# Kernel optimization log

Hardware: AMD Instinct MI355X
Metric: run time of the kernel (lower is better)

Reference implementation:

```python
import jax, jax.numpy as jnp
import numpy as np

N, C, H, W = 4, 256, 64, 64
D = 128  # inter_channels = C // 2


def setup_inputs() -> dict:
    key = jax.random.key(0)
    ks = jax.random.split(key, 9)
    s = 0.05  # weight scale
    return {
        "x": jax.random.normal(ks[0], (N, C, H, W), jnp.float32),
        "Wg": jax.random.normal(ks[1], (D, C), jnp.float32) * s,
        "bg": jax.random.normal(ks[2], (D,), jnp.float32) * s,
        "Wt": jax.random.normal(ks[3], (D, C), jnp.float32) * s,
        "bt": jax.random.normal(ks[4], (D,), jnp.float32) * s,
        "Wp": jax.random.normal(ks[5], (D, C), jnp.float32) * s,
        "bp": jax.random.normal(ks[6], (D,), jnp.float32) * s,
        "Wz": jax.random.normal(ks[7], (C, D), jnp.float32) * s,
        "bz": jax.random.normal(ks[8], (C,), jnp.float32) * s,
    }


def reference(x, Wg, bg, Wt, bt, Wp, bp, Wz, bz):
    # NonLocalBlock, mode='embedded', dimension=2, bn_layer=False.
    # 1x1 convs are per-pixel linear maps over channels.
    n, c, h, w = x.shape
    xf = x.reshape(n, c, h * w)                                  # (N,C,S)
    g_x = jnp.einsum('dc,ncs->nds', Wg, xf) + bg[None, :, None]  # (N,D,S)
    th = jnp.einsum('dc,ncs->nds', Wt, xf) + bt[None, :, None]   # (N,D,S)
    ph = jnp.einsum('dc,ncs->nds', Wp, xf) + bp[None, :, None]   # (N,D,S)
    f = jnp.einsum('nds,ndt->nst', th, ph)                       # (N,S,S)
    att = jax.nn.softmax(f, axis=-1)
    y = jnp.einsum('nst,ndt->nds', att, g_x)                     # (N,D,S)
    w_y = jnp.einsum('cd,nds->ncs', Wz, y) + bz[None, :, None]   # (N,C,S)
    return (w_y + xf).reshape(n, c, h, w)
```

## Files before the change

### kernel.cpp

```cpp
#include <hip/hip_runtime.h>
#include <math.h>

#define N_ 4
#define C_ 256
#define D_ 128
#define S_ 4096
#define LOG2E 1.4426950408889634f
#define SPLIT 4
#define TPS 16

typedef __attribute__((ext_vector_type(4))) float f32x4;
typedef __attribute__((ext_vector_type(16))) float f32x16;
typedef __attribute__((ext_vector_type(8))) short short8;
typedef __attribute__((ext_vector_type(8))) unsigned short ushort8;
typedef __attribute__((ext_vector_type(4))) unsigned short ushort4v;

#define MFMA16(a, b, c) __builtin_amdgcn_mfma_f32_16x16x32_bf16((a), (b), (c), 0, 0, 0)
#define MFMA32(a, b, c) __builtin_amdgcn_mfma_f32_32x32x16_bf16((a), (b), (c), 0, 0, 0)

__device__ __forceinline__ unsigned short f2bf(float f) {
  union { float f; unsigned int u; } v; v.f = f;
  unsigned int r = v.u + 0x7fffu + ((v.u >> 16) & 1u);
  return (unsigned short)(r >> 16);
}
__device__ __forceinline__ float bf2f(unsigned short u) {
  union { unsigned int u; float f; } v; v.u = ((unsigned int)u) << 16;
  return v.f;
}
__device__ __forceinline__ unsigned cvtpk(float lo, float hi) {
  unsigned r;
  asm("v_cvt_pk_bf16_f32 %0, %1, %2" : "=v"(r) : "v"(lo), "v"(hi));
  return r;
}
__device__ __forceinline__ float vsum16(const f32x16& v) {
  float a = (v[0] + v[1]) + (v[2] + v[3]);
  float b = (v[4] + v[5]) + (v[6] + v[7]);
  float c = (v[8] + v[9]) + (v[10] + v[11]);
  float d = (v[12] + v[13]) + (v[14] + v[15]);
  return (a + b) + (c + d);
}
__device__ __forceinline__ void gload16(const void* g, void* l) {
  __builtin_amdgcn_global_load_lds((const __attribute__((address_space(1))) unsigned int*)g,
                                   (__attribute__((address_space(3))) unsigned int*)l,
                                   16, 0, 0);
}

__global__ void k_convw(const float* __restrict__ w0, const float* __restrict__ w1,
                        const float* __restrict__ w2, const float* __restrict__ w3,
                        unsigned short* __restrict__ d0, unsigned short* __restrict__ d1,
                        unsigned short* __restrict__ d2, unsigned short* __restrict__ d3) {
  int b = blockIdx.x;
  int w = b >> 4;
  int i = (b & 15) * 256 + threadIdx.x;
  const float* s = (w == 0) ? w0 : (w == 1) ? w1 : (w == 2) ? w2 : w3;
  unsigned short* d = (w == 0) ? d0 : (w == 1) ? d1 : (w == 2) ? d2 : d3;
  const float4* sp = reinterpret_cast<const float4*>(s) + (size_t)i * 2;
  float4 a = sp[0], c = sp[1];
  ushort8 o;
  o[0] = f2bf(a.x); o[1] = f2bf(a.y); o[2] = f2bf(a.z); o[3] = f2bf(a.w);
  o[4] = f2bf(c.x); o[5] = f2bf(c.y); o[6] = f2bf(c.z); o[7] = f2bf(c.w);
  reinterpret_cast<ushort8*>(d)[i] = o;
}

__global__ __launch_bounds__(256, 3) void k_proj(
    const float* __restrict__ x,
    const unsigned short* __restrict__ wg, const unsigned short* __restrict__ wt,
    const unsigned short* __restrict__ wp,
    const float* __restrict__ bg, const float* __restrict__ bt, const float* __restrict__ bp,
    unsigned short* __restrict__ qb, unsigned short* __restrict__ kb, unsigned short* __restrict__ vb)
{
  __shared__ __align__(16) unsigned short xs[C_ * 64];
  const int tid = threadIdx.x;
  const int p = blockIdx.x >> 8;
  const int n = (blockIdx.x >> 6) & 3;
  const int s0 = (blockIdx.x & 63) << 6;
  const float* xsrc = x + (size_t)n * C_ * S_ + s0;
#pragma unroll
  for (int i = 0; i < 16; ++i) {
    int ch = i * 256 + tid;
    int c = ch >> 4, s4 = (ch & 15) << 2;
    float4 v = *reinterpret_cast<const float4*>(xsrc + (size_t)c * S_ + s4);
    ushort4v o;
    o[0] = f2bf(v.x); o[1] = f2bf(v.y); o[2] = f2bf(v.z); o[3] = f2bf(v.w);
    *reinterpret_cast<ushort4v*>(xs + c * 64 + s4) = o;
  }
  __syncthreads();
  const int lane = tid & 63, wid = tid >> 6;
  const int l15 = lane & 15, g = lane >> 4;
  const int scol = wid * 16 + l15;

  short8 bx[8];
#pragma unroll
  for (int kc = 0; kc < 8; ++kc) {
    int cb = kc * 32 + g * 8;
    short8 t;
#pragma unroll
    for (int j = 0; j < 8; ++j) t[j] = (short)xs[(cb + j) * 64 + scol];
    bx[kc] = t;
  }

  const unsigned short* W = (p == 0) ? wg : ((p == 1) ? wt : wp);
  const float* bias = (p == 0) ? bg : ((p == 1) ? bt : bp);
  const float osc = (p == 1) ? LOG2E : 1.0f;
  const f32x4 fz = {0.f, 0.f, 0.f, 0.f};
  f32x4 acc[8];
#pragma unroll
  for (int dt = 0; dt < 8; ++dt) acc[dt] = fz;
#pragma unroll
  for (int dt = 0; dt < 8; ++dt) {
    const unsigned short* wrow = W + (size_t)(dt * 16 + l15) * C_ + g * 8;
#pragma unroll
    for (int kc = 0; kc < 8; ++kc) {
      short8 a = *reinterpret_cast<const short8*>(wrow + kc * 32);
      acc[dt] = MFMA16(a, bx[kc], acc[dt]);
    }
  }
  if (p == 0) {
#pragma unroll
    for (int dt = 0; dt < 8; ++dt) {
#pragma unroll
      for (int r = 0; r < 4; ++r) {
        int d = dt * 16 + 4 * g + r;
        vb[((size_t)n * D_ + d) * S_ + s0 + scol] = f2bf(acc[dt][r] + bias[d]);
      }
    }
  } else {
    unsigned short* dst = (p == 1) ? qb : kb;
    unsigned short* row = dst + ((size_t)(n * S_) + s0 + scol) * D_;
#pragma unroll
    for (int dt = 0; dt < 8; ++dt) {
      ushort4v o;
#pragma unroll
      for (int r = 0; r < 4; ++r)
        o[r] = f2bf((acc[dt][r] + bias[dt * 16 + 4 * g + r]) * osc);
      *reinterpret_cast<ushort4v*>(row + dt * 16 + 4 * g) = o;
    }
  }
}

__global__ __launch_bounds__(512, 2) void k_attn(
    const unsigned short* __restrict__ qb, const unsigned short* __restrict__ kb,
    const unsigned short* __restrict__ vb,
    unsigned short* __restrict__ opart, float2* __restrict__ ml)
{
  __shared__ __align__(16) unsigned short ksm[2][64 * 128];
  __shared__ __align__(16) unsigned short vsm[2][128 * 64];
  const int tid = threadIdx.x, lane = tid & 63, w = tid >> 6;
  const int qw = w & 3, hw = w >> 2;
  const int l31 = lane & 31, hi = lane >> 5;
  const int b = blockIdx.x;
  const int sp = b & 3, qt = (b >> 2) & 31, n = b >> 7;
  const int q0 = qt << 7;

  unsigned koff[2], voff[2], ubo[2];
#pragma unroll
  for (int j = 0; j < 2; ++j) {
    int f = j * 512 + tid;
    int kr = f >> 4, kc = f & 15;
    koff[j] = kr * D_ + ((kc ^ (kr & 7)) << 3);
    int vr = f >> 3, vc = f & 7;
    voff[j] = vr * S_ + ((vc ^ (vr & 7)) << 3);
    ubo[j] = (unsigned)(j * 512 + (tid & 448)) * 8;
  }
  const unsigned short* kb0 = kb + ((size_t)n * S_ + (size_t)sp * TPS * 64) * D_;
  const unsigned short* vb0 = vb + (size_t)n * D_ * S_ + sp * TPS * 64;

  auto stage = [&](int buf, int t) {
    const unsigned short* kt = kb0 + (size_t)t * 64 * D_;
    const unsigned short* vt = vb0 + t * 64;
#pragma unroll
    for (int j = 0; j < 2; ++j) gload16(kt + koff[j], &ksm[buf][ubo[j]]);
#pragma unroll
    for (int j = 0; j < 2; ++j) gload16(vt + voff[j], &vsm[buf][ubo[j]]);
  };

  stage(0, 0);

  const unsigned short* qsrc = qb + ((size_t)(n * S_) + q0 + qw * 32 + l31) * D_;
  short8 qf[8];
#pragma unroll
  for (int k = 0; k < 8; ++k)
    qf[k] = *reinterpret_cast<const short8*>(qsrc + k * 16 + hi * 8);

  const f32x16 z16 = {0.f,0.f,0.f,0.f,0.f,0.f,0.f,0.f,0.f,0.f,0.f,0.f,0.f,0.f,0.f,0.f};
  f32x16 oacc[4];
#pragma unroll
  for (int db = 0; db < 4; ++db) oacc[db] = z16;
  float l_ = 0.f;

  __syncthreads();
  int cur = 0;

  for (int t = 0; t < TPS; ++t) {
    if (t + 1 < TPS) stage(cur ^ 1, t + 1);

    const unsigned short* ksb = ksm[cur];
    const unsigned short* vsb = vsm[cur];

    f32x16 pA = z16;
    __builtin_amdgcn_s_setprio(1);
#pragma unroll
    for (int ks = 0; ks < 8; ++ks) {
      int c = ks * 2 + hi;
      int r0 = hw * 32 + l31;
      short8 k0 = *reinterpret_cast<const short8*>(ksb + r0 * 128 + ((c ^ (r0 & 7)) << 3));
      pA = MFMA32(k0, qf[ks], pA);
    }
    __builtin_amdgcn_s_setprio(0);

#pragma unroll
    for (int i = 0; i < 16; ++i) pA[i] = exp2f(pA[i]);
    l_ += vsum16(pA);

    short8 pa[2];
#pragma unroll
    for (int ks = 0; ks < 2; ++ks) {
      int ba = ks * 8;
      unsigned u0 = cvtpk(pA[ba + 0], pA[ba + 1]);
      unsigned u1 = cvtpk(pA[ba + 2], pA[ba + 3]);
      unsigned u2 = cvtpk(pA[ba + 4], pA[ba + 5]);
      unsigned u3 = cvtpk(pA[ba + 6], pA[ba + 7]);
      asm("v_permlane32_swap_b32 %0, %1" : "+v"(u0), "+v"(u2));
      asm("v_permlane32_swap_b32 %0, %1" : "+v"(u1), "+v"(u3));
      union { unsigned u[4]; short8 s; } mm;
      mm.u[0] = u0; mm.u[1] = u1; mm.u[2] = u2; mm.u[3] = u3;
      pa[ks] = mm.s;
    }

    __builtin_amdgcn_s_setprio(1);
#pragma unroll
    for (int ks = 0; ks < 2; ++ks) {
      int cc = hw * 4 + ks * 2 + hi;
#pragma unroll
      for (int db = 0; db < 4; ++db) {
        int r = db * 32 + l31;
        short8 v = *reinterpret_cast<const short8*>(vsb + r * 64 + ((cc ^ (r & 7)) << 3));
        oacc[db] = MFMA32(pa[ks], v, oacc[db]);
      }
    }
    __builtin_amdgcn_s_setprio(0);

    __syncthreads();
    cur ^= 1;
  }

  float lrow = l_ + __shfl_xor(l_, 32);
  float* msm = (float*)(&ksm[0][0]);
  float* lsm = (float*)(&vsm[0][0]);
  __syncthreads();
  if (hw == 1) {
#pragma unroll
    for (int db = 0; db < 2; ++db)
#pragma unroll
      for (int reg = 0; reg < 16; ++reg)
        msm[(db * 16 + reg) * 256 + qw * 64 + lane] = oacc[db][reg];
    lsm[qw * 64 + lane] = lrow;
  }
  __syncthreads();
  if (hw == 0) {
#pragma unroll
    for (int db = 0; db < 2; ++db)
#pragma unroll
      for (int reg = 0; reg < 16; ++reg)
        oacc[db][reg] += msm[(db * 16 + reg) * 256 + qw * 64 + lane];
    lrow += lsm[qw * 64 + lane];
  }
  __syncthreads();
  if (hw == 1) {
#pragma unroll
    for (int db = 2; db < 4; ++db)
#pragma unroll
      for (int reg = 0; reg < 16; ++reg)
        msm[((db - 2) * 16 + reg) * 256 + qw * 64 + lane] = oacc[db][reg];
  }
  __syncthreads();
  if (hw == 0) {
#pragma unroll
    for (int db = 2; db < 4; ++db)
#pragma unroll
      for (int reg = 0; reg < 16; ++reg)
        oacc[db][reg] += msm[((db - 2) * 16 + reg) * 256 + qw * 64 + lane];

    float linv = 1.f / lrow;
    unsigned short* ob = opart + (((size_t)(n * SPLIT + sp)) * S_ + q0 + qw * 32) * D_;
#pragma unroll
    for (int reg = 0; reg < 16; ++reg) {
      int rr = (reg & 3) + 8 * (reg >> 2) + 4 * hi;
      float li = __shfl(linv, rr);
#pragma unroll
      for (int db = 0; db < 4; ++db)
        ob[(size_t)rr * D_ + db * 32 + l31] = f2bf(oacc[db][reg] * li);
    }
    if (hi == 0) {
      ml[((size_t)(n * SPLIT + sp)) * S_ + q0 + qw * 32 + l31] = make_float2(0.f, lrow);
    }
  }
}

__global__ __launch_bounds__(256, 2) void k_final(
    const unsigned short* __restrict__ opart, const float2* __restrict__ ml,
    const unsigned short* __restrict__ wz, const float* __restrict__ bz,
    const float* __restrict__ x, float* __restrict__ out)
{
  __shared__ __align__(16) unsigned short ysm[32 * 128];
  __shared__ float wsm[32][4];
  const int tid = threadIdx.x, lane = tid & 63, wid = tid >> 6;
  const int l15 = lane & 15, g = lane >> 4;
  const int n = blockIdx.x >> 7, s0 = (blockIdx.x & 127) << 5;

  if (tid < 32) {
    int row = s0 + tid;
    float mv[4], lv[4];
    float M = -3.4e38f;
#pragma unroll
    for (int i = 0; i < 4; ++i) {
      float2 v = ml[(size_t)(n * 4 + i) * S_ + row];
      mv[i] = v.x; lv[i] = v.y;
      M = fmaxf(M, mv[i]);
    }
    float wsum = 0.f, wv[4];
#pragma unroll
    for (int i = 0; i < 4; ++i) { wv[i] = lv[i] * exp2f((mv[i] - M) * LOG2E); wsum += wv[i]; }
    float L = 1.f / wsum;
#pragma unroll
    for (int i = 0; i < 4; ++i) wsm[tid][i] = wv[i] * L;
  }
  __syncthreads();

#pragma unroll
  for (int i = 0; i < 2; ++i) {
    int ch = i * 256 + tid;
    int row = ch >> 4, d8 = ch & 15;
    const unsigned short* p = opart + ((size_t)(n * 4) * S_ + s0 + row) * D_ + d8 * 8;
    float acc[8] = {0.f, 0.f, 0.f, 0.f, 0.f, 0.f, 0.f, 0.f};
#pragma unroll
    for (int j = 0; j < 4; ++j) {
      ushort8 a = *reinterpret_cast<const ushort8*>(p + (size_t)j * S_ * D_);
      float wj = wsm[row][j];
#pragma unroll
      for (int e = 0; e < 8; ++e) acc[e] += bf2f(a[e]) * wj;
    }
    ushort8 o;
#pragma unroll
    for (int e = 0; e < 8; ++e) o[e] = f2bf(acc[e]);
    *reinterpret_cast<ushort8*>(ysm + row * 128 + ((d8 ^ (row & 7)) << 3)) = o;
  }
  __syncthreads();

  const int c0 = wid * 64;
  const f32x4 fz = {0.f, 0.f, 0.f, 0.f};
  f32x4 acc[4][2];
#pragma unroll
  for (int ct = 0; ct < 4; ++ct)
#pragma unroll
    for (int st = 0; st < 2; ++st) acc[ct][st] = fz;
#pragma unroll
  for (int kc = 0; kc < 4; ++kc) {
    short8 by[2];
#pragma unroll
    for (int st = 0; st < 2; ++st) {
      int r = st * 16 + l15;
      int ch = (kc * 4 + g) ^ (r & 7);
      by[st] = *reinterpret_cast<const short8*>(ysm + r * 128 + ch * 8);
    }
#pragma unroll
    for (int ct = 0; ct < 4; ++ct) {
      const short8 aw = *reinterpret_cast<const short8*>(
          wz + (size_t)(c0 + ct * 16 + l15) * D_ + kc * 32 + g * 8);
#pragma unroll
      for (int st = 0; st < 2; ++st) acc[ct][st] = MFMA16(aw, by[st], acc[ct][st]);
    }
  }
#pragma unroll
  for (int ct = 0; ct < 4; ++ct)
#pragma unroll
    for (int r = 0; r < 4; ++r) {
      int c = c0 + ct * 16 + 4 * g + r;
      float bias = bz[c];
#pragma unroll
      for (int st = 0; st < 2; ++st) {
        int s = s0 + st * 16 + l15;
        size_t idx = ((size_t)(n * C_ + c)) * S_ + s;
        out[idx] = acc[ct][st][r] + bias + x[idx];
      }
    }
}

extern "C" void kernel_launch(void* const* d_in, const int* in_sizes, int n_in,
                              void* d_out, int out_size, void* d_ws, size_t ws_size,
                              hipStream_t stream) {
  const float* x  = (const float*)d_in[0];
  const float* Wg = (const float*)d_in[1];
  const float* bg = (const float*)d_in[2];
  const float* Wt = (const float*)d_in[3];
  const float* bt = (const float*)d_in[4];
  const float* Wp = (const float*)d_in[5];
  const float* bp = (const float*)d_in[6];
  const float* Wz = (const float*)d_in[7];
  const float* bz = (const float*)d_in[8];
  float* out = (float*)d_out;
  char* ws = (char*)d_ws;
  const size_t MB = 1u << 20;
  unsigned short* qb    = (unsigned short*)(ws);
  unsigned short* kb    = (unsigned short*)(ws + 4 * MB);
  unsigned short* vb    = (unsigned short*)(ws + 8 * MB);
  unsigned short* opart = (unsigned short*)(ws + 12 * MB);
  float2*        mlbuf  = (float2*)(ws + 28 * MB);
  unsigned short* wgb   = (unsigned short*)(ws + 28 * MB + 524288);
  unsigned short* wtb   = (unsigned short*)(ws + 28 * MB + 524288 + 65536);
  unsigned short* wpb   = (unsigned short*)(ws + 28 * MB + 524288 + 131072);
  unsigned short* wzb   = (unsigned short*)(ws + 28 * MB + 524288 + 196608);

  k_convw<<<64, 256, 0, stream>>>(Wg, Wt, Wp, Wz, wgb, wtb, wpb, wzb);
  k_proj <<<768, 256, 0, stream>>>(x, wgb, wtb, wpb, bg, bt, bp, qb, kb, vb);
  k_attn <<<512, 512, 0, stream>>>(qb, kb, vb, opart, mlbuf);
  k_final<<<512, 256, 0, stream>>>(opart, mlbuf, wzb, bz, x, out);
}
```

Baseline: 106.1 us.

## Restructure attention so each wave owns 64 query rows, raise KV split to 8

The attention kernel now gives each wave two 32-row query tiles that share each K/V fragment read from LDS. This doubles MFMA work per LDS load and removes the cross-wave LDS reduction of partial outputs. The KV sequence is split 8 ways with 8 tiles each, giving a grid of 256 blocks, and the final kernel merges 8 partials with a simplified weighting that drops the max-rescale. Risks are higher register pressure from the doubled accumulators under launch_bounds(512,2), fewer blocks in flight, and more partial-output traffic for the final kernel to read.

Result: slower. 164.4 us (+54.9%).

```diff
diff --git a/kernel.cpp b/kernel.cpp
--- a/kernel.cpp
+++ b/kernel.cpp
@@ -6,8 +6,8 @@
 #define D_ 128
 #define S_ 4096
 #define LOG2E 1.4426950408889634f
-#define SPLIT 4
-#define TPS 16
+#define SPLIT 8
+#define TPS 8
 
 typedef __attribute__((ext_vector_type(4))) float f32x4;
 typedef __attribute__((ext_vector_type(16))) float f32x16;
@@ -146,11 +146,10 @@
   __shared__ __align__(16) unsigned short ksm[2][64 * 128];
   __shared__ __align__(16) unsigned short vsm[2][128 * 64];
   const int tid = threadIdx.x, lane = tid & 63, w = tid >> 6;
-  const int qw = w & 3, hw = w >> 2;
   const int l31 = lane & 31, hi = lane >> 5;
   const int b = blockIdx.x;
-  const int sp = b & 3, qt = (b >> 2) & 31, n = b >> 7;
-  const int q0 = qt << 7;
+  const int sp = b & 7, n = (b >> 3) & 3, qt = b >> 5;
+  const int q0 = qt * 512 + w * 64;
 
   unsigned koff[2], voff[2], ubo[2];
 #pragma unroll
@@ -162,8 +161,8 @@
     voff[j] = vr * S_ + ((vc ^ (vr & 7)) << 3);
     ubo[j] = (unsigned)(j * 512 + (tid & 448)) * 8;
   }
-  const unsigned short* kb0 = kb + ((size_t)n * S_ + (size_t)sp * TPS * 64) * D_;
-  const unsigned short* vb0 = vb + (size_t)n * D_ * S_ + sp * TPS * 64;
+  const unsigned short* kb0 = kb + ((size_t)n * S_ + sp * 512) * D_;
+  const unsigned short* vb0 = vb + (size_t)n * D_ * S_ + sp * 512;
 
   auto stage = [&](int buf, int t) {
     const unsigned short* kt = kb0 + (size_t)t * 64 * D_;
@@ -176,17 +175,20 @@
 
   stage(0, 0);
 
-  const unsigned short* qsrc = qb + ((size_t)(n * S_) + q0 + qw * 32 + l31) * D_;
-  short8 qf[8];
-#pragma unroll
-  for (int k = 0; k < 8; ++k)
-    qf[k] = *reinterpret_cast<const short8*>(qsrc + k * 16 + hi * 8);
+  const unsigned short* qsrcA = qb + ((size_t)(n * S_) + q0 + l31) * D_;
+  const unsigned short* qsrcB = qsrcA + (size_t)32 * D_;
+  short8 qfA[8], qfB[8];
+#pragma unroll
+  for (int k = 0; k < 8; ++k) {
+    qfA[k] = *reinterpret_cast<const short8*>(qsrcA + k * 16 + hi * 8);
+    qfB[k] = *reinterpret_cast<const short8*>(qsrcB + k * 16 + hi * 8);
+  }
 
   const f32x16 z16 = {0.f,0.f,0.f,0.f,0.f,0.f,0.f,0.f,0.f,0.f,0.f,0.f,0.f,0.f,0.f,0.f};
-  f32x16 oacc[4];
-#pragma unroll
-  for (int db = 0; db < 4; ++db) oacc[db] = z16;
-  float l_ = 0.f;
+  f32x16 oaccA[4], oaccB[4];
+#pragma unroll
+  for (int db = 0; db < 4; ++db) { oaccA[db] = z16; oaccB[db] = z16; }
+  float lA = 0.f, lB = 0.f;
 
   __syncthreads();
   int cur = 0;
@@ -197,103 +199,94 @@
     const unsigned short* ksb = ksm[cur];
     const unsigned short* vsb = vsm[cur];
 
-    f32x16 pA = z16;
-    __builtin_amdgcn_s_setprio(1);
-#pragma unroll
-    for (int ks = 0; ks < 8; ++ks) {
-      int c = ks * 2 + hi;
-      int r0 = hw * 32 + l31;
-      short8 k0 = *reinterpret_cast<const short8*>(ksb + r0 * 128 + ((c ^ (r0 & 7)) << 3));
-      pA = MFMA32(k0, qf[ks], pA);
-    }
-    __builtin_amdgcn_s_setprio(0);
-
-#pragma unroll
-    for (int i = 0; i < 16; ++i) pA[i] = exp2f(pA[i]);
-    l_ += vsum16(pA);
-
-    short8 pa[2];
-#pragma unroll
-    for (int ks = 0; ks < 2; ++ks) {
-      int ba = ks * 8;
-      unsigned u0 = cvtpk(pA[ba + 0], pA[ba + 1]);
-      unsigned u1 = cvtpk(pA[ba + 2], pA[ba + 3]);
-      unsigned u2 = cvtpk(pA[ba + 4], pA[ba + 5]);
-      unsigned u3 = cvtpk(pA[ba + 6], pA[ba + 7]);
-      asm("v_permlane32_swap_b32 %0, %1" : "+v"(u0), "+v"(u2));
-      asm("v_permlane32_swap_b32 %0, %1" : "+v"(u1), "+v"(u3));
-      union { unsigned u[4]; short8 s; } mm;
-      mm.u[0] = u0; mm.u[1] = u1; mm.u[2] = u2; mm.u[3] = u3;
-      pa[ks] = mm.s;
-    }
-
-    __builtin_amdgcn_s_setprio(1);
-#pragma unroll
-    for (int ks = 0; ks < 2; ++ks) {
-      int cc = hw * 4 + ks * 2 + hi;
-#pragma unroll
-      for (int db = 0; db < 4; ++db) {
-        int r = db * 32 + l31;
-        short8 v = *reinterpret_cast<const short8*>(vsb + r * 64 + ((cc ^ (r & 7)) << 3));
-        oacc[db] = MFMA32(pa[ks], v, oacc[db]);
+#pragma unroll
+    for (int h = 0; h < 2; ++h) {
+      f32x16 pA = z16, pB = z16;
+      __builtin_amdgcn_s_setprio(1);
+#pragma unroll
+      for (int ks = 0; ks < 8; ++ks) {
+        int c = ks * 2 + hi;
+        int r = h * 32 + l31;
+        short8 k0 = *reinterpret_cast<const short8*>(ksb + r * 128 + ((c ^ (r & 7)) << 3));
+        pA = MFMA32(k0, qfA[ks], pA);
+        pB = MFMA32(k0, qfB[ks], pB);
       }
-    }
-    __builtin_amdgcn_s_setprio(0);
+      __builtin_amdgcn_s_setprio(0);
+
+#pragma unroll
+      for (int i = 0; i < 16; ++i) pA[i] = exp2f(pA[i]);
+#pragma unroll
+      for (int i = 0; i < 16; ++i) pB[i] = exp2f(pB[i]);
+      lA += vsum16(pA);
+      lB += vsum16(pB);
+
+      short8 paA[2], paB[2];
+#pragma unroll
+      for (int ksl = 0; ksl < 2; ++ksl) {
+        int ba = ksl * 8;
+        {
+          unsigned u0 = cvtpk(pA[ba + 0], pA[ba + 1]);
+          unsigned u1 = cvtpk(pA[ba + 2], pA[ba + 3]);
+          unsigned u2 = cvtpk(pA[ba + 4], pA[ba + 5]);
+          unsigned u3 = cvtpk(pA[ba + 6], pA[ba + 7]);
+          asm("v_permlane32_swap_b32 %0, %1" : "+v"(u0), "+v"(u2));
+          asm("v_permlane32_swap_b32 %0, %1" : "+v"(u1), "+v"(u3));
+          union { unsigned u[4]; short8 s; } mm;
+          mm.u[0] = u0; mm.u[1] = u1; mm.u[2] = u2; mm.u[3] = u3;
+          paA[ksl] = mm.s;
+        }
+        {
+          unsigned u0 = cvtpk(pB[ba + 0], pB[ba + 1]);
+          unsigned u1 = cvtpk(pB[ba + 2], pB[ba + 3]);
+          unsigned u2 = cvtpk(pB[ba + 4], pB[ba + 5]);
+          unsigned u3 = cvtpk(pB[ba + 6], pB[ba + 7]);
+          asm("v_permlane32_swap_b32 %0, %1" : "+v"(u0), "+v"(u2));
+          asm("v_permlane32_swap_b32 %0, %1" : "+v"(u1), "+v"(u3));
+          union { unsigned u[4]; short8 s; } mm;
+          mm.u[0] = u0; mm.u[1] = u1; mm.u[2] = u2; mm.u[3] = u3;
+          paB[ksl] = mm.s;
+        }
+      }
+
+      __builtin_amdgcn_s_setprio(1);
+#pragma unroll
+      for (int ksl = 0; ksl < 2; ++ksl) {
+        int cc = (2 * h + ksl) * 2 + hi;
+#pragma unroll
+        for (int db = 0; db < 4; ++db) {
+          int r = db * 32 + l31;
+          short8 v = *reinterpret_cast<const short8*>(vsb + r * 64 + ((cc ^ (r & 7)) << 3));
+          oaccA[db] = MFMA32(paA[ksl], v, oaccA[db]);
+          oaccB[db] = MFMA32(paB[ksl], v, oaccB[db]);
+        }
+      }
+      __builtin_amdgcn_s_setprio(0);
+    }
 
     __syncthreads();
     cur ^= 1;
   }
 
-  float lrow = l_ + __shfl_xor(l_, 32);
-  float* msm = (float*)(&ksm[0][0]);
-  float* lsm = (float*)(&vsm[0][0]);
-  __syncthreads();
-  if (hw == 1) {
-#pragma unroll
-    for (int db = 0; db < 2; ++db)
-#pragma unroll
-      for (int reg = 0; reg < 16; ++reg)
-        msm[(db * 16 + reg) * 256 + qw * 64 + lane] = oacc[db][reg];
-    lsm[qw * 64 + lane] = lrow;
-  }
-  __syncthreads();
-  if (hw == 0) {
-#pragma unroll
-    for (int db = 0; db < 2; ++db)
-#pragma unroll
-      for (int reg = 0; reg < 16; ++reg)
-        oacc[db][reg] += msm[(db * 16 + reg) * 256 + qw * 64 + lane];
-    lrow += lsm[qw * 64 + lane];
-  }
-  __syncthreads();
-  if (hw == 1) {
-#pragma unroll
-    for (int db = 2; db < 4; ++db)
-#pragma unroll
-      for (int reg = 0; reg < 16; ++reg)
-        msm[((db - 2) * 16 + reg) * 256 + qw * 64 + lane] = oacc[db][reg];
-  }
-  __syncthreads();
-  if (hw == 0) {
-#pragma unroll
-    for (int db = 2; db < 4; ++db)
-#pragma unroll
-      for (int reg = 0; reg < 16; ++reg)
-        oacc[db][reg] += msm[((db - 2) * 16 + reg) * 256 + qw * 64 + lane];
-
-    float linv = 1.f / lrow;
-    unsigned short* ob = opart + (((size_t)(n * SPLIT + sp)) * S_ + q0 + qw * 32) * D_;
-#pragma unroll
-    for (int reg = 0; reg < 16; ++reg) {
-      int rr = (reg & 3) + 8 * (reg >> 2) + 4 * hi;
-      float li = __shfl(linv, rr);
-#pragma unroll
-      for (int db = 0; db < 4; ++db)
-        ob[(size_t)rr * D_ + db * 32 + l31] = f2bf(oacc[db][reg] * li);
-    }
-    if (hi == 0) {
-      ml[((size_t)(n * SPLIT + sp)) * S_ + q0 + qw * 32 + l31] = make_float2(0.f, lrow);
-    }
+  float lrowA = lA + __shfl_xor(lA, 32);
+  float lrowB = lB + __shfl_xor(lB, 32);
+  float linvA = 1.f / lrowA, linvB = 1.f / lrowB;
+  unsigned short* obA = opart + (((size_t)(n * SPLIT + sp)) * S_ + q0) * D_;
+  unsigned short* obB = obA + (size_t)32 * D_;
+#pragma unroll
+  for (int reg = 0; reg < 16; ++reg) {
+    int rr = (reg & 3) + 8 * (reg >> 2) + 4 * hi;
+    float liA = __shfl(linvA, rr);
+    float liB = __shfl(linvB, rr);
+#pragma unroll
+    for (int db = 0; db < 4; ++db) {
+      obA[(size_t)rr * D_ + db * 32 + l31] = f2bf(oaccA[db][reg] * liA);
+      obB[(size_t)rr * D_ + db * 32 + l31] = f2bf(oaccB[db][reg] * liB);
+    }
+  }
+  if (hi == 0) {
+    float2* mlp = ml + ((size_t)(n * SPLIT + sp)) * S_ + q0;
+    mlp[l31] = make_float2(0.f, lrowA);
+    mlp[32 + l31] = make_float2(0.f, lrowB);
   }
 }
 
@@ -303,27 +296,23 @@
     const float* __restrict__ x, float* __restrict__ out)
 {
   __shared__ __align__(16) unsigned short ysm[32 * 128];
-  __shared__ float wsm[32][4];
+  __shared__ float wsm[32][8];
   const int tid = threadIdx.x, lane = tid & 63, wid = tid >> 6;
   const int l15 = lane & 15, g = lane >> 4;
   const int n = blockIdx.x >> 7, s0 = (blockIdx.x & 127) << 5;
 
   if (tid < 32) {
     int row = s0 + tid;
-    float mv[4], lv[4];
-    float M = -3.4e38f;
-#pragma unroll
-    for (int i = 0; i < 4; ++i) {
-      float2 v = ml[(size_t)(n * 4 + i) * S_ + row];
-      mv[i] = v.x; lv[i] = v.y;
-      M = fmaxf(M, mv[i]);
-    }
-    float wsum = 0.f, wv[4];
-#pragma unroll
-    for (int i = 0; i < 4; ++i) { wv[i] = lv[i] * exp2f((mv[i] - M) * LOG2E); wsum += wv[i]; }
+    float wv[8], wsum = 0.f;
+#pragma unroll
+    for (int i = 0; i < 8; ++i) {
+      float2 v = ml[(size_t)(n * 8 + i) * S_ + row];
+      wv[i] = v.y;
+      wsum += wv[i];
+    }
     float L = 1.f / wsum;
 #pragma unroll
-    for (int i = 0; i < 4; ++i) wsm[tid][i] = wv[i] * L;
+    for (int i = 0; i < 8; ++i) wsm[tid][i] = wv[i] * L;
   }
   __syncthreads();
 
@@ -331,10 +320,10 @@
   for (int i = 0; i < 2; ++i) {
     int ch = i * 256 + tid;
     int row = ch >> 4, d8 = ch & 15;
-    const unsigned short* p = opart + ((size_t)(n * 4) * S_ + s0 + row) * D_ + d8 * 8;
+    const unsigned short* p = opart + ((size_t)(n * 8) * S_ + s0 + row) * D_ + d8 * 8;
     float acc[8] = {0.f, 0.f, 0.f, 0.f, 0.f, 0.f, 0.f, 0.f};
 #pragma unroll
-    for (int j = 0; j < 4; ++j) {
+    for (int j = 0; j < 8; ++j) {
       ushort8 a = *reinterpret_cast<const ushort8*>(p + (size_t)j * S_ * D_);
       float wj = wsm[row][j];
 #pragma unroll
@@ -405,14 +394,14 @@
   unsigned short* kb    = (unsigned short*)(ws + 4 * MB);
   unsigned short* vb    = (unsigned short*)(ws + 8 * MB);
   unsigned short* opart = (unsigned short*)(ws + 12 * MB);
-  float2*        mlbuf  = (float2*)(ws + 28 * MB);
-  unsigned short* wgb   = (unsigned short*)(ws + 28 * MB + 524288);
-  unsigned short* wtb   = (unsigned short*)(ws + 28 * MB + 524288 + 65536);
-  unsigned short* wpb   = (unsigned short*)(ws + 28 * MB + 524288 + 131072);
-  unsigned short* wzb   = (unsigned short*)(ws + 28 * MB + 524288 + 196608);
+  float2*        mlbuf  = (float2*)(ws + 44 * MB);
+  unsigned short* wgb   = (unsigned short*)(ws + 45 * MB);
+  unsigned short* wtb   = (unsigned short*)(ws + 45 * MB + 65536);
+  unsigned short* wpb   = (unsigned short*)(ws + 45 * MB + 131072);
+  unsigned short* wzb   = (unsigned short*)(ws + 45 * MB + 196608);
 
   k_convw<<<64, 256, 0, stream>>>(Wg, Wt, Wp, Wz, wgb, wtb, wpb, wzb);
   k_proj <<<768, 256, 0, stream>>>(x, wgb, wtb, wpb, bg, bt, bp, qb, kb, vb);
-  k_attn <<<512, 512, 0, stream>>>(qb, kb, vb, opart, mlbuf);
+  k_attn <<<256, 512, 0, stream>>>(qb, kb, vb, opart, mlbuf);
   k_final<<<512, 256, 0, stream>>>(opart, mlbuf, wzb, bz, x, out);
 }
```
